# Performance work log

Hardware: AMD Instinct MI355X
Metric: run time of the kernel (lower is better)

Reference implementation:

```python
import jax, jax.numpy as jnp
import numpy as np

B, S, D, H, MLP = 8, 1024, 768, 12, 3072
HD = D // H
EPS = 1e-5


def setup_inputs() -> dict:
    key = jax.random.key(0)
    ks = jax.random.split(key, 5)
    sd = lambda fan_in: 1.0 / np.sqrt(fan_in)
    return {
        "x": jax.random.normal(ks[0], (B, S, D), jnp.float32),
        "w_qkv": jax.random.normal(ks[1], (D, 3 * D), jnp.float32) * sd(D),
        "w_out": jax.random.normal(ks[2], (D, D), jnp.float32) * sd(D),
        "b_out": jnp.zeros((D,), jnp.float32),
        "w1": jax.random.normal(ks[3], (D, MLP), jnp.float32) * sd(D),
        "b1": jnp.zeros((MLP,), jnp.float32),
        "w2": jax.random.normal(ks[4], (MLP, D), jnp.float32) * sd(MLP),
        "b2": jnp.zeros((D,), jnp.float32),
    }


def _instance_norm(x):
    # torch InstanceNorm2d on a 3D [B,S,D] tensor treats it as unbatched (C,H,W):
    # normalize over (S, D) per batch element, biased var, eps=1e-5, no affine.
    mu = jnp.mean(x, axis=(1, 2), keepdims=True)
    var = jnp.mean(jnp.square(x - mu), axis=(1, 2), keepdims=True)
    return (x - mu) * jax.lax.rsqrt(var + EPS)


def reference(x, w_qkv, w_out, b_out, w1, b1, w2, b2):
    scale = HD ** -0.5
    # --- self-attention branch ---
    h = _instance_norm(x)
    qkv = (h @ w_qkv).reshape(B, S, 3, H, HD)          # (qkv, heads, head_dim) split
    qkv = qkv.transpose(2, 0, 3, 1, 4)                  # [3, B, H, S, HD]
    q, k, v = qkv[0], qkv[1], qkv[2]
    att = jax.nn.softmax(jnp.einsum('bhxd,bhyd->bhxy', q, k) * scale, axis=-1)
    o = jnp.einsum('bhxy,bhyd->bhxd', att, v)           # [B, H, S, HD]
    o = o.transpose(0, 2, 1, 3).reshape(B, S, D)        # b h l d -> b l (h d)
    x = x + (o @ w_out + b_out)
    # --- MLP branch (exact erf GELU, as nn.GELU default) ---
    h2 = _instance_norm(x)
    m = jax.nn.gelu(h2 @ w1 + b1, approximate=False) @ w2 + b2
    return x + m
```

## Files before the change

kernel.cpp:

```cpp
#include <hip/hip_runtime.h>
#include <hip/hip_bf16.h>

typedef __hip_bfloat16 bf16;
typedef __attribute__((ext_vector_type(8))) short short8;
typedef __attribute__((ext_vector_type(4))) float f32x4;

#define B_   8
#define S_   1024
#define D_   768
#define H_   12
#define HD_  64
#define MLP_ 3072
#define SD_  (S_ * D_)

#define QSCALE 0.18033688011112042f

__device__ __forceinline__ void gl2lds16(const bf16* g, bf16* l) {
  __builtin_amdgcn_global_load_lds(
      (const __attribute__((address_space(1))) unsigned*)(const void*)g,
      (__attribute__((address_space(3))) unsigned*)(void*)l, 16, 0, 0);
}

__global__ __launch_bounds__(256) void transpose_all(
    const float* __restrict__ w_qkv, const float* __restrict__ w_out,
    const float* __restrict__ w1, const float* __restrict__ w2,
    bf16* __restrict__ t_qkv, bf16* __restrict__ t_out,
    bf16* __restrict__ t1, bf16* __restrict__ t2) {
  const int t = blockIdx.x;
  const float* in; bf16* out; int R, C, idx;
  if (t < 1728)      { in = w_qkv; out = t_qkv; R = 768;  C = 2304; idx = t; }
  else if (t < 2304) { in = w_out; out = t_out; R = 768;  C = 768;  idx = t - 1728; }
  else if (t < 4608) { in = w1;    out = t1;    R = 768;  C = 3072; idx = t - 2304; }
  else               { in = w2;    out = t2;    R = 3072; C = 768;  idx = t - 4608; }
  const int nbx = C >> 5;
  const int bx = (idx % nbx) * 32, by = (idx / nbx) * 32;
  __shared__ float tt[32][33];
  const int tx = threadIdx.x & 31, ty = threadIdx.x >> 5;
#pragma unroll
  for (int rr = 0; rr < 32; rr += 8)
    tt[ty + rr][tx] = in[(long)(by + ty + rr) * C + bx + tx];
  __syncthreads();
#pragma unroll
  for (int rr = 0; rr < 32; rr += 8)
    out[(long)(bx + ty + rr) * R + by + tx] = __float2bfloat16(tt[tx][ty + rr]);
}

__global__ __launch_bounds__(256) void stats_partial(const float* __restrict__ x,
                                                     float* __restrict__ redp) {
  const long off = (long)blockIdx.x * 8192;
  float s = 0.f, s2 = 0.f;
#pragma unroll
  for (int it = 0; it < 8; ++it) {
    float4 v = *(const float4*)(x + off + ((long)threadIdx.x + it * 256) * 4);
    s += v.x + v.y + v.z + v.w;
    s2 += v.x * v.x + v.y * v.y + v.z * v.z + v.w * v.w;
  }
#pragma unroll
  for (int o = 1; o < 64; o <<= 1) { s += __shfl_xor(s, o, 64); s2 += __shfl_xor(s2, o, 64); }
  __shared__ float sh[8];
  const int wave = threadIdx.x >> 6, lane = threadIdx.x & 63;
  if (lane == 0) { sh[wave * 2] = s; sh[wave * 2 + 1] = s2; }
  __syncthreads();
  if (threadIdx.x == 0) {
    redp[blockIdx.x * 2]     = sh[0] + sh[2] + sh[4] + sh[6];
    redp[blockIdx.x * 2 + 1] = sh[1] + sh[3] + sh[5] + sh[7];
  }
}

__global__ __launch_bounds__(512) void stats_final(const float* __restrict__ redp,
                                                   float* __restrict__ red_x,
                                                   float* __restrict__ red2) {
  const int b = threadIdx.x >> 6, lane = threadIdx.x & 63;
  const int i0 = (b * 96 + lane) * 2;
  float s  = redp[i0]     + ((lane < 32) ? redp[i0 + 128]     : 0.f);
  float s2 = redp[i0 + 1] + ((lane < 32) ? redp[i0 + 128 + 1] : 0.f);
#pragma unroll
  for (int o = 1; o < 64; o <<= 1) { s += __shfl_xor(s, o, 64); s2 += __shfl_xor(s2, o, 64); }
  if (lane == 0) { red_x[b * 2] = s; red_x[b * 2 + 1] = s2; }
  if (threadIdx.x < 16) red2[threadIdx.x] = 0.f;
}

__global__ __launch_bounds__(256) void norm_k(const float* __restrict__ x,
                                              const float* __restrict__ sums,
                                              bf16* __restrict__ h) {
  const long i = ((long)blockIdx.x * 256 + threadIdx.x) * 8;
  const int b = (int)(i / SD_);
  const float mu = sums[b * 2] * (1.0f / SD_);
  const float var = sums[b * 2 + 1] * (1.0f / SD_) - mu * mu;
  const float rs = rsqrtf(var + 1e-5f);
  float4 v0 = *(const float4*)(x + i);
  float4 v1 = *(const float4*)(x + i + 4);
  __align__(16) bf16 tmp[8];
  tmp[0] = __float2bfloat16((v0.x - mu) * rs);
  tmp[1] = __float2bfloat16((v0.y - mu) * rs);
  tmp[2] = __float2bfloat16((v0.z - mu) * rs);
  tmp[3] = __float2bfloat16((v0.w - mu) * rs);
  tmp[4] = __float2bfloat16((v1.x - mu) * rs);
  tmp[5] = __float2bfloat16((v1.y - mu) * rs);
  tmp[6] = __float2bfloat16((v1.z - mu) * rs);
  tmp[7] = __float2bfloat16((v1.w - mu) * rs);
  *(short8*)(h + i) = *(const short8*)tmp;
}

template <int EPI, int TN, bool STATS>
__global__ __launch_bounds__(256) void gemm128(
    const bf16* __restrict__ A, const bf16* __restrict__ Bt,
    int M, int N, int K,
    const float* __restrict__ biasf, const float* __restrict__ resf,
    float* __restrict__ outf,
    bf16* __restrict__ outb0, bf16* __restrict__ outb1, bf16* __restrict__ outb2,
    float* __restrict__ statp) {
  constexpr int J = TN / 32;
  __shared__ __align__(16) bf16 As[2][128 * 32];
  __shared__ __align__(16) bf16 Bs[2][TN * 32];
  __shared__ float sred[8];
  const int tid = threadIdx.x;
  const int bm = blockIdx.x * 128, bn = blockIdx.y * TN;
  const int wave = tid >> 6, lane = tid & 63;
  const int quad = lane >> 4, l16 = lane & 15;
  const int wm = (wave >> 1) << 6, wn = (wave & 1) * (TN / 2);

  f32x4 acc[4][J];
#pragma unroll
  for (int i = 0; i < 4; ++i)
#pragma unroll
    for (int j = 0; j < J; ++j) acc[i][j] = (f32x4){0.f, 0.f, 0.f, 0.f};

  const int srow = tid >> 2;
  const int scol = (tid & 3) * 8;
  const bf16* Ab = A + (long)(bm + srow) * K + scol;
  const bf16* Bb = Bt + (long)(bn + srow) * K + scol;
  const long rowK64 = (long)64 * K;

  auto stage = [&](int buf, int k0) {
    gl2lds16(Ab + k0, &As[buf][0] + tid * 8);
    gl2lds16(Ab + rowK64 + k0, &As[buf][0] + 2048 + tid * 8);
    gl2lds16(Bb + k0, &Bs[buf][0] + tid * 8);
    if (TN == 128) gl2lds16(Bb + rowK64 + k0, &Bs[buf][0] + 2048 + tid * 8);
  };

  stage(0, 0);
  const int nk = K >> 5;
  for (int kt = 0; kt < nk; ++kt) {
    const int cur = kt & 1;
    __syncthreads();
    if (kt + 1 < nk) stage(cur ^ 1, (kt + 1) * 32);
    short8 a[4], b[J];
#pragma unroll
    for (int i = 0; i < 4; ++i)
      a[i] = *(const short8*)(&As[cur][0] + (wm + i * 16 + l16) * 32 + quad * 8);
#pragma unroll
    for (int j = 0; j < J; ++j)
      b[j] = *(const short8*)(&Bs[cur][0] + (wn + j * 16 + l16) * 32 + quad * 8);
#pragma unroll
    for (int i = 0; i < 4; ++i)
#pragma unroll
      for (int j = 0; j < J; ++j)
        acc[i][j] = __builtin_amdgcn_mfma_f32_16x16x32_bf16(a[i], b[j], acc[i][j], 0, 0, 0);
  }

  const int m0 = bm + wm + quad * 4;
  const int n0 = bn + wn + l16;
  float ts = 0.f, ts2 = 0.f;
#pragma unroll
  for (int i = 0; i < 4; ++i) {
#pragma unroll
    for (int j = 0; j < J; ++j) {
      const int n = n0 + j * 16;
#pragma unroll
      for (int r = 0; r < 4; ++r) {
        const int m = m0 + i * 16 + r;
        float v = acc[i][j][r];
        if (EPI == 0) {
          const int t = n / D_;
          const int rr2 = n - t * D_;
          const int hh = rr2 >> 6, dd = rr2 & 63;
          const int bb = m >> 10, ss = m & 1023;
          const long hoff = (long)(bb * H_ + hh);
          if (t == 0)      outb0[(hoff * S_ + ss) * HD_ + dd] = __float2bfloat16(v * QSCALE);
          else if (t == 1) outb1[(hoff * S_ + ss) * HD_ + dd] = __float2bfloat16(v);
          else             outb2[(hoff * HD_ + dd) * S_ + ss] = __float2bfloat16(v);
        } else if (EPI == 1) {
          v += biasf[n] + resf[(long)m * N + n];
          outf[(long)m * N + n] = v;
          if (STATS) { ts += v; ts2 += v * v; }
        } else {
          v += biasf[n];
          float u = v * v;
          float y = v * (1.0f + 0.044715f * u) * 0.7978845608028654f;
          float z = exp2f(y * -2.885390081777927f);
          v = v * __builtin_amdgcn_rcpf(1.0f + z);
          outb0[(long)m * N + n] = __float2bfloat16(v);
        }
      }
    }
  }
  if (STATS) {
#pragma unroll
    for (int o = 1; o < 64; o <<= 1) { ts += __shfl_xor(ts, o, 64); ts2 += __shfl_xor(ts2, o, 64); }
    if (lane == 0) { sred[wave * 2] = ts; sred[wave * 2 + 1] = ts2; }
    __syncthreads();
    if (tid == 0) {
      const int batch = bm >> 10;
      atomicAdd(&statp[batch * 2], sred[0] + sred[2] + sred[4] + sred[6]);
      atomicAdd(&statp[batch * 2 + 1], sred[1] + sred[3] + sred[5] + sred[7]);
    }
  }
}

__global__ __launch_bounds__(256) void attn64(const bf16* __restrict__ q,
                                              const bf16* __restrict__ k,
                                              const bf16* __restrict__ vt,
                                              bf16* __restrict__ o) {
  __shared__ __align__(16) bf16 Ks[2][64 * 64];
  __shared__ __align__(16) bf16 Vs[2][64 * 64];
  __shared__ __align__(16) bf16 Ps[4 * 16 * 64];
  const int bh = blockIdx.x, qt = blockIdx.y;
  const int tid = threadIdx.x, wave = tid >> 6, lane = tid & 63;
  const int quad = lane >> 4, l16 = lane & 15;
  const int sw = (l16 & 7) ^ ((l16 >> 3) & 1);
  const long base = (long)bh * (S_ * HD_);
  const bf16* kg = k + base;
  const bf16* vg = vt + base;

  const int srow = tid >> 3;
  const int scg = (tid & 7) ^ (srow & 7) ^ ((srow >> 3) & 1);

  short8 aq[2];
#pragma unroll
  for (int kk = 0; kk < 2; ++kk)
    aq[kk] = *(const short8*)(q + base + (long)(qt * 64 + wave * 16 + l16) * HD_ +
                              kk * 32 + quad * 8);

  gl2lds16(kg + (long)srow * HD_ + scg * 8, &Ks[0][0] + tid * 8);
  gl2lds16(kg + (long)(32 + srow) * HD_ + scg * 8, &Ks[0][0] + 2048 + tid * 8);
  gl2lds16(vg + (long)srow * S_ + scg * 8, &Vs[0][0] + tid * 8);
  gl2lds16(vg + (long)(32 + srow) * S_ + scg * 8, &Vs[0][0] + 2048 + tid * 8);

  f32x4 oacc[4];
#pragma unroll
  for (int j = 0; j < 4; ++j) oacc[j] = (f32x4){0.f, 0.f, 0.f, 0.f};
  float lp[4] = {0.f, 0.f, 0.f, 0.f};

  for (int c = 0; c < 16; ++c) {
    const int cur = c & 1;
    __syncthreads();

    f32x4 s[4];
#pragma unroll
    for (int nj = 0; nj < 4; ++nj) s[nj] = (f32x4){0.f, 0.f, 0.f, 0.f};
#pragma unroll
    for (int kk = 0; kk < 2; ++kk) {
#pragma unroll
      for (int nj = 0; nj < 4; ++nj) {
        short8 bk = *(const short8*)(&Ks[cur][0] + (nj * 16 + l16) * 64 +
                                     (((kk * 4 + quad) ^ sw) * 8));
        s[nj] = __builtin_amdgcn_mfma_f32_16x16x32_bf16(aq[kk], bk, s[nj], 0, 0, 0);
      }
    }

    if (c < 15) {
      const int nxt = cur ^ 1;
      gl2lds16(kg + (long)((c + 1) * 64 + srow) * HD_ + scg * 8, &Ks[nxt][0] + tid * 8);
      gl2lds16(kg + (long)((c + 1) * 64 + 32 + srow) * HD_ + scg * 8, &Ks[nxt][0] + 2048 + tid * 8);
      gl2lds16(vg + (long)srow * S_ + (c + 1) * 64 + scg * 8, &Vs[nxt][0] + tid * 8);
      gl2lds16(vg + (long)(32 + srow) * S_ + (c + 1) * 64 + scg * 8, &Vs[nxt][0] + 2048 + tid * 8);
    }

#pragma unroll
    for (int r = 0; r < 4; ++r) {
      const int row = quad * 4 + r;
      const int swp = (row & 7) ^ ((row >> 3) & 1);
#pragma unroll
      for (int nj = 0; nj < 4; ++nj) {
        float p = exp2f(s[nj][r]);
        lp[r] += p;
        const int chunk = nj * 2 + (l16 >> 3);
        Ps[wave * 1024 + row * 64 + ((chunk ^ swp) * 8) + (l16 & 7)] =
            __float2bfloat16(p);
      }
    }

#pragma unroll
    for (int kk = 0; kk < 2; ++kk) {
      short8 ap = *(const short8*)(Ps + wave * 1024 + l16 * 64 +
                                   (((kk * 4 + quad) ^ sw) * 8));
#pragma unroll
      for (int dj = 0; dj < 4; ++dj) {
        short8 bv = *(const short8*)(&Vs[cur][0] + (dj * 16 + l16) * 64 +
                                     (((kk * 4 + quad) ^ sw) * 8));
        oacc[dj] = __builtin_amdgcn_mfma_f32_16x16x32_bf16(ap, bv, oacc[dj], 0, 0, 0);
      }
    }
  }

  const int b = bh / H_, hh = bh - b * H_;
#pragma unroll
  for (int r = 0; r < 4; ++r) {
    float l = lp[r];
#pragma unroll
    for (int off = 1; off < 16; off <<= 1) l += __shfl_xor(l, off, 64);
    const int sg = qt * 64 + wave * 16 + quad * 4 + r;
    const float inv = 1.0f / l;
    const long rowoff = ((long)b * S_ + sg) * D_ + hh * HD_;
#pragma unroll
    for (int dj = 0; dj < 4; ++dj)
      o[rowoff + dj * 16 + l16] = __float2bfloat16(oacc[dj][r] * inv);
  }
}

extern "C" void kernel_launch(void* const* d_in, const int* in_sizes, int n_in,
                              void* d_out, int out_size, void* d_ws, size_t ws_size,
                              hipStream_t stream) {
  const float* x     = (const float*)d_in[0];
  const float* w_qkv = (const float*)d_in[1];
  const float* w_out = (const float*)d_in[2];
  const float* b_out = (const float*)d_in[3];
  const float* w1    = (const float*)d_in[4];
  const float* b1    = (const float*)d_in[5];
  const float* w2    = (const float*)d_in[6];
  const float* b2    = (const float*)d_in[7];
  float* out = (float*)d_out;

  bf16* wt_qkv = (bf16*)d_ws;
  bf16* wt_out = wt_qkv + 2304 * 768;
  bf16* wt1    = wt_out + 768 * 768;
  bf16* wt2    = wt1 + 3072 * 768;
  bf16* qb     = wt2 + 768 * 3072;
  bf16* kb     = qb + 6291456;
  bf16* vtb    = kb + 6291456;
  bf16* ob     = vtb + 6291456;
  float* x1f   = (float*)(ob + 6291456);
  bf16* hb     = (bf16*)(x1f + 6291456);
  float* redp  = (float*)(hb + 6291456);
  float* red_x = redp + 1536;
  float* red2  = red_x + 16;
  bf16* gb     = qb;

  transpose_all<<<6912, 256, 0, stream>>>(w_qkv, w_out, w1, w2, wt_qkv, wt_out, wt1, wt2);

  stats_partial<<<B_ * 96, 256, 0, stream>>>(x, redp);
  stats_final<<<1, 512, 0, stream>>>(redp, red_x, red2);
  norm_k<<<3072, 256, 0, stream>>>(x, red_x, hb);

  gemm128<0, 128, false><<<dim3(64, 18), 256, 0, stream>>>(
      hb, wt_qkv, 8192, 2304, 768, nullptr, nullptr, nullptr, qb, kb, vtb, nullptr);
  attn64<<<dim3(B_ * H_, 16), 256, 0, stream>>>(qb, kb, vtb, ob);

  gemm128<1, 64, true><<<dim3(64, 12), 256, 0, stream>>>(
      ob, wt_out, 8192, 768, 768, b_out, x, x1f, nullptr, nullptr, nullptr, red2);
  norm_k<<<3072, 256, 0, stream>>>(x1f, red2, hb);

  gemm128<2, 128, false><<<dim3(64, 24), 256, 0, stream>>>(
      hb, wt1, 8192, 3072, 768, b1, nullptr, nullptr, gb, nullptr, nullptr, nullptr);
  gemm128<1, 64, false><<<dim3(64, 12), 256, 0, stream>>>(
      gb, wt2, 8192, 768, 3072, b2, x1f, out, nullptr, nullptr, nullptr, nullptr);
}
```

Measured before the change: 378.7 us.

## Fold second instance norm into MLP GEMM epilogue and retile GEMM to 128x64x64

Drops the second norm kernel. The out-projection GEMM now also writes a bf16 copy of x1, and the first MLP GEMM applies the normalisation algebraically in its epilogue as rs*(acc - mu*colsum(w1)) + b1. The w1 column sums are computed by extra blocks in the transpose kernel. Separately, the GEMM changes from 128x128/128x64 tiles with K-step 32 to 128x64 tiles with K-step 64 and an XOR-swizzled LDS layout to reduce bank conflicts. Risks are precision loss from applying the norm to the raw bf16 x1 rather than to normalised values, and more blocks with less reuse per tile in the QKV and MLP1 GEMMs.

New measurement: 401.4 us. 1.06x slower.

```diff
diff --git a/kernel.cpp b/kernel.cpp
--- a/kernel.cpp
+++ b/kernel.cpp
@@ -25,8 +25,19 @@
     const float* __restrict__ w_qkv, const float* __restrict__ w_out,
     const float* __restrict__ w1, const float* __restrict__ w2,
     bf16* __restrict__ t_qkv, bf16* __restrict__ t_out,
-    bf16* __restrict__ t1, bf16* __restrict__ t2) {
+    bf16* __restrict__ t1, bf16* __restrict__ t2,
+    float* __restrict__ cs1) {
   const int t = blockIdx.x;
+  if (t >= 6912) {
+    const int n = (t - 6912) * 256 + threadIdx.x;
+    float s = 0.f;
+    for (int k0 = 0; k0 < 768; k0 += 8) {
+#pragma unroll
+      for (int u = 0; u < 8; ++u) s += w1[(long)(k0 + u) * 3072 + n];
+    }
+    cs1[n] = s;
+    return;
+  }
   const float* in; bf16* out; int R, C, idx;
   if (t < 1728)      { in = w_qkv; out = t_qkv; R = 768;  C = 2304; idx = t; }
   else if (t < 2304) { in = w_out; out = t_out; R = 768;  C = 768;  idx = t - 1728; }
@@ -102,70 +113,85 @@
   *(short8*)(h + i) = *(const short8*)tmp;
 }
 
-template <int EPI, int TN, bool STATS>
-__global__ __launch_bounds__(256) void gemm128(
+template <int EPI, bool STATS>
+__global__ __launch_bounds__(256) void gemm_k(
     const bf16* __restrict__ A, const bf16* __restrict__ Bt,
     int M, int N, int K,
     const float* __restrict__ biasf, const float* __restrict__ resf,
+    const float* __restrict__ cs, const float* __restrict__ stat_in,
     float* __restrict__ outf,
     bf16* __restrict__ outb0, bf16* __restrict__ outb1, bf16* __restrict__ outb2,
     float* __restrict__ statp) {
-  constexpr int J = TN / 32;
-  __shared__ __align__(16) bf16 As[2][128 * 32];
-  __shared__ __align__(16) bf16 Bs[2][TN * 32];
+  __shared__ __align__(16) bf16 As[2][128 * 64];
+  __shared__ __align__(16) bf16 Bs[2][64 * 64];
   __shared__ float sred[8];
   const int tid = threadIdx.x;
-  const int bm = blockIdx.x * 128, bn = blockIdx.y * TN;
+  const int bm = blockIdx.x * 128, bn = blockIdx.y * 64;
   const int wave = tid >> 6, lane = tid & 63;
   const int quad = lane >> 4, l16 = lane & 15;
-  const int wm = (wave >> 1) << 6, wn = (wave & 1) * (TN / 2);
-
-  f32x4 acc[4][J];
+  const int wm = (wave >> 1) * 64, wn = (wave & 1) * 32;
+  const int swz = l16 & 7;
+
+  f32x4 acc[4][2];
 #pragma unroll
   for (int i = 0; i < 4; ++i)
 #pragma unroll
-    for (int j = 0; j < J; ++j) acc[i][j] = (f32x4){0.f, 0.f, 0.f, 0.f};
-
-  const int srow = tid >> 2;
-  const int scol = (tid & 3) * 8;
-  const bf16* Ab = A + (long)(bm + srow) * K + scol;
-  const bf16* Bb = Bt + (long)(bn + srow) * K + scol;
-  const long rowK64 = (long)64 * K;
+    for (int j = 0; j < 2; ++j) acc[i][j] = (f32x4){0.f, 0.f, 0.f, 0.f};
+
+  const int srow = tid >> 3;
+  const int sgc = (tid & 7) ^ (srow & 7);
+  const bf16* Ab = A + (long)(bm + srow) * K + sgc * 8;
+  const bf16* Bb = Bt + (long)(bn + srow) * K + sgc * 8;
 
   auto stage = [&](int buf, int k0) {
-    gl2lds16(Ab + k0, &As[buf][0] + tid * 8);
-    gl2lds16(Ab + rowK64 + k0, &As[buf][0] + 2048 + tid * 8);
-    gl2lds16(Bb + k0, &Bs[buf][0] + tid * 8);
-    if (TN == 128) gl2lds16(Bb + rowK64 + k0, &Bs[buf][0] + 2048 + tid * 8);
+#pragma unroll
+    for (int s = 0; s < 4; ++s)
+      gl2lds16(Ab + (long)(s * 32) * K + k0, &As[buf][0] + s * 2048 + tid * 8);
+#pragma unroll
+    for (int s = 0; s < 2; ++s)
+      gl2lds16(Bb + (long)(s * 32) * K + k0, &Bs[buf][0] + s * 2048 + tid * 8);
   };
 
   stage(0, 0);
-  const int nk = K >> 5;
+  const int nk = K >> 6;
   for (int kt = 0; kt < nk; ++kt) {
     const int cur = kt & 1;
     __syncthreads();
-    if (kt + 1 < nk) stage(cur ^ 1, (kt + 1) * 32);
-    short8 a[4], b[J];
-#pragma unroll
-    for (int i = 0; i < 4; ++i)
-      a[i] = *(const short8*)(&As[cur][0] + (wm + i * 16 + l16) * 32 + quad * 8);
-#pragma unroll
-    for (int j = 0; j < J; ++j)
-      b[j] = *(const short8*)(&Bs[cur][0] + (wn + j * 16 + l16) * 32 + quad * 8);
-#pragma unroll
-    for (int i = 0; i < 4; ++i)
-#pragma unroll
-      for (int j = 0; j < J; ++j)
-        acc[i][j] = __builtin_amdgcn_mfma_f32_16x16x32_bf16(a[i], b[j], acc[i][j], 0, 0, 0);
+    if (kt + 1 < nk) stage(cur ^ 1, (kt + 1) * 64);
+    short8 a[2][4], b[2][2];
+#pragma unroll
+    for (int kk = 0; kk < 2; ++kk) {
+      const int co = ((kk * 4 + quad) ^ swz) * 8;
+#pragma unroll
+      for (int i = 0; i < 4; ++i)
+        a[kk][i] = *(const short8*)(&As[cur][0] + (wm + i * 16 + l16) * 64 + co);
+#pragma unroll
+      for (int j = 0; j < 2; ++j)
+        b[kk][j] = *(const short8*)(&Bs[cur][0] + (wn + j * 16 + l16) * 64 + co);
+    }
+#pragma unroll
+    for (int kk = 0; kk < 2; ++kk)
+#pragma unroll
+      for (int i = 0; i < 4; ++i)
+#pragma unroll
+        for (int j = 0; j < 2; ++j)
+          acc[i][j] = __builtin_amdgcn_mfma_f32_16x16x32_bf16(a[kk][i], b[kk][j], acc[i][j], 0, 0, 0);
   }
 
   const int m0 = bm + wm + quad * 4;
   const int n0 = bn + wn + l16;
+  const int batch = bm >> 10;
+  float mu = 0.f, rs = 0.f;
+  if (EPI == 2) {
+    const float s1 = stat_in[batch * 2], s2v = stat_in[batch * 2 + 1];
+    mu = s1 * (1.0f / SD_);
+    rs = rsqrtf(s2v * (1.0f / SD_) - mu * mu + 1e-5f);
+  }
   float ts = 0.f, ts2 = 0.f;
 #pragma unroll
   for (int i = 0; i < 4; ++i) {
 #pragma unroll
-    for (int j = 0; j < J; ++j) {
+    for (int j = 0; j < 2; ++j) {
       const int n = n0 + j * 16;
 #pragma unroll
       for (int r = 0; r < 4; ++r) {
@@ -183,14 +209,18 @@
         } else if (EPI == 1) {
           v += biasf[n] + resf[(long)m * N + n];
           outf[(long)m * N + n] = v;
+          outb0[(long)m * N + n] = __float2bfloat16(v);
           if (STATS) { ts += v; ts2 += v * v; }
-        } else {
-          v += biasf[n];
+        } else if (EPI == 2) {
+          v = rs * (v - mu * cs[n]) + biasf[n];
           float u = v * v;
           float y = v * (1.0f + 0.044715f * u) * 0.7978845608028654f;
           float z = exp2f(y * -2.885390081777927f);
           v = v * __builtin_amdgcn_rcpf(1.0f + z);
           outb0[(long)m * N + n] = __float2bfloat16(v);
+        } else {
+          v += biasf[n] + resf[(long)m * N + n];
+          outf[(long)m * N + n] = v;
         }
       }
     }
@@ -201,7 +231,6 @@
     if (lane == 0) { sred[wave * 2] = ts; sred[wave * 2 + 1] = ts2; }
     __syncthreads();
     if (tid == 0) {
-      const int batch = bm >> 10;
       atomicAdd(&statp[batch * 2], sred[0] + sred[2] + sred[4] + sred[6]);
       atomicAdd(&statp[batch * 2 + 1], sred[1] + sred[3] + sred[5] + sred[7]);
     }
@@ -335,24 +364,31 @@
   float* redp  = (float*)(hb + 6291456);
   float* red_x = redp + 1536;
   float* red2  = red_x + 16;
+  float* cs1   = red2 + 16;
   bf16* gb     = qb;
-
-  transpose_all<<<6912, 256, 0, stream>>>(w_qkv, w_out, w1, w2, wt_qkv, wt_out, wt1, wt2);
+  bf16* x1b    = hb;
+
+  transpose_all<<<6924, 256, 0, stream>>>(w_qkv, w_out, w1, w2,
+                                          wt_qkv, wt_out, wt1, wt2, cs1);
 
   stats_partial<<<B_ * 96, 256, 0, stream>>>(x, redp);
   stats_final<<<1, 512, 0, stream>>>(redp, red_x, red2);
   norm_k<<<3072, 256, 0, stream>>>(x, red_x, hb);
 
-  gemm128<0, 128, false><<<dim3(64, 18), 256, 0, stream>>>(
-      hb, wt_qkv, 8192, 2304, 768, nullptr, nullptr, nullptr, qb, kb, vtb, nullptr);
+  gemm_k<0, false><<<dim3(64, 36), 256, 0, stream>>>(
+      hb, wt_qkv, 8192, 2304, 768, nullptr, nullptr, nullptr, nullptr,
+      nullptr, qb, kb, vtb, nullptr);
   attn64<<<dim3(B_ * H_, 16), 256, 0, stream>>>(qb, kb, vtb, ob);
 
-  gemm128<1, 64, true><<<dim3(64, 12), 256, 0, stream>>>(
-      ob, wt_out, 8192, 768, 768, b_out, x, x1f, nullptr, nullptr, nullptr, red2);
-  norm_k<<<3072, 256, 0, stream>>>(x1f, red2, hb);
-
-  gemm128<2, 128, false><<<dim3(64, 24), 256, 0, stream>>>(
-      hb, wt1, 8192, 3072, 768, b1, nullptr, nullptr, gb, nullptr, nullptr, nullptr);
-  gemm128<1, 64, false><<<dim3(64, 12), 256, 0, stream>>>(
-      gb, wt2, 8192, 768, 3072, b2, x1f, out, nullptr, nullptr, nullptr, nullptr);
-}
+  gemm_k<1, true><<<dim3(64, 12), 256, 0, stream>>>(
+      ob, wt_out, 8192, 768, 768, b_out, x, nullptr, nullptr,
+      x1f, x1b, nullptr, nullptr, red2);
+
+  gemm_k<2, false><<<dim3(64, 48), 256, 0, stream>>>(
+      x1b, wt1, 8192, 3072, 768, b1, nullptr, cs1, red2,
+      nullptr, gb, nullptr, nullptr, nullptr);
+
+  gemm_k<3, false><<<dim3(64, 12), 256, 0, stream>>>(
+      gb, wt2, 8192, 768, 3072, b2, x1f, nullptr, nullptr,
+      out, nullptr, nullptr, nullptr, nullptr);
+}
```
